# Kernel optimization log

Measured on AMD Instinct MI355X. Metric: run time of the kernel, lower is better.

The kernel has to match this reference:

```python
import jax, jax.numpy as jnp
import numpy as np

N = 100000   # nodes
E = 1600000  # edges
DIN, DH, DOUT = 64, 128, 128


def setup_inputs() -> dict:
    key = jax.random.key(0)
    ks = jax.random.split(key, 12)
    x = jax.random.normal(ks[0], (N, DIN), dtype=jnp.float32)
    edge_index = jax.random.randint(ks[1], (2, E), 0, N, dtype=jnp.int32)
    s = 1.0 / np.sqrt(DIN)
    W1 = jax.random.uniform(ks[2], (DIN, DH), jnp.float32, -s, s)
    b1 = jnp.zeros((DH,), jnp.float32)
    g1 = jnp.ones((DH,), jnp.float32)
    bt1 = jnp.zeros((DH,), jnp.float32)
    s2 = 1.0 / np.sqrt(DH)
    W2 = jax.random.uniform(ks[3], (DH, DOUT), jnp.float32, -s2, s2)
    b2 = jnp.zeros((DOUT,), jnp.float32)
    g2 = jnp.ones((DOUT,), jnp.float32)
    bt2 = jnp.zeros((DOUT,), jnp.float32)
    return {"x": x, "edge_index": edge_index, "W1": W1, "b1": b1, "g1": g1,
            "bt1": bt1, "W2": W2, "b2": b2, "g2": g2, "bt2": bt2}


def _layer_norm(h, g, b, eps=1e-5):
    mu = h.mean(-1, keepdims=True)
    var = h.var(-1, keepdims=True)
    return (h - mu) * jax.lax.rsqrt(var + eps) * g + b


def reference(x, edge_index, W1, b1, g1, bt1, W2, b2, g2, bt2):
    # GCN normalization with self-loops (shared graph structure for both layers)
    src, dst = edge_index[0], edge_index[1]
    loops = jnp.arange(N, dtype=src.dtype)
    src = jnp.concatenate([src, loops])
    dst = jnp.concatenate([dst, loops])
    deg = jax.ops.segment_sum(jnp.ones_like(src, jnp.float32), dst, num_segments=N)
    dinv = jnp.where(deg > 0, jax.lax.rsqrt(deg), 0.0)
    norm = dinv[src] * dinv[dst]  # [E+N]

    def gcn(h, W, b):
        hw = h @ W                         # linear first (PyG GCNConv)
        msg = hw[src] * norm[:, None]      # gather + edge scale
        return jax.ops.segment_sum(msg, dst, num_segments=N) + b

    h = jax.nn.relu(_layer_norm(gcn(x, W1, b1), g1, bt1))
    # dropout is identity at inference
    h = jax.nn.relu(_layer_norm(gcn(h, W2, b2), g2, bt2))
    return h
```

## Files before the change

### kernel.cpp

```cpp
#include <hip/hip_runtime.h>

#define NN 100000
#define NE 1600000
#define NBKT 196
#define CAP 12288
#define EPB 8192
#define ABLK ((NE + EPB - 1) / EPB)
typedef unsigned short u16;
typedef unsigned int u32;

typedef __attribute__((ext_vector_type(8))) short short8v;
typedef __attribute__((ext_vector_type(4))) float f32x4;

__device__ __forceinline__ u32 f2bf(float f) {
    u32 u = __float_as_uint(f);
    return (u + 0x7fffu + ((u >> 16) & 1u)) >> 16;
}
__device__ __forceinline__ u32 pack2(float a, float b) {
    return f2bf(a) | (f2bf(b) << 16);
}
__device__ __forceinline__ void accum8(float* a, uint4 u, float w) {
    a[0] += __uint_as_float(u.x << 16) * w;
    a[1] += __uint_as_float(u.x & 0xffff0000u) * w;
    a[2] += __uint_as_float(u.y << 16) * w;
    a[3] += __uint_as_float(u.y & 0xffff0000u) * w;
    a[4] += __uint_as_float(u.z << 16) * w;
    a[5] += __uint_as_float(u.z & 0xffff0000u) * w;
    a[6] += __uint_as_float(u.w << 16) * w;
    a[7] += __uint_as_float(u.w & 0xffff0000u) * w;
}

__global__ __launch_bounds__(256) void kA_bin(const int* __restrict__ src,
                                              const int* __restrict__ dst,
                                              int* __restrict__ gcnt,
                                              u32* __restrict__ binned) {
    __shared__ int bc[NBKT];
    __shared__ int cbase[NBKT];
    const int tid = threadIdx.x;
    for (int i = tid; i < NBKT; i += 256) bc[i] = 0;
    __syncthreads();
    const int e0 = blockIdx.x * EPB;
#pragma unroll
    for (int i = 0; i < EPB / 256; ++i) {
        const int e = e0 + i * 256 + tid;
        if (e < NE) atomicAdd(&bc[dst[e] >> 9], 1);
    }
    __syncthreads();
    for (int i = tid; i < NBKT; i += 256)
        cbase[i] = bc[i] ? atomicAdd(&gcnt[i], bc[i]) : 0;
    __syncthreads();
    for (int i = tid; i < NBKT; i += 256) bc[i] = 0;
    __syncthreads();
#pragma unroll
    for (int i = 0; i < EPB / 256; ++i) {
        const int e = e0 + i * 256 + tid;
        if (e < NE) {
            const int d = dst[e];
            const int bkt = d >> 9;
            const int p = atomicAdd(&bc[bkt], 1);
            binned[bkt * CAP + cbase[bkt] + p] = ((u32)src[e] << 9) | (u32)(d & 511);
        }
    }
}

__global__ __launch_bounds__(256) void kB_fill(const u32* __restrict__ binned,
                                               const int* __restrict__ gcnt,
                                               int2* __restrict__ off2,
                                               float* __restrict__ dinv,
                                               int* __restrict__ csr) {
    __shared__ int lcnt[512];
    __shared__ int lpos[512];
    __shared__ int ws[4];
    const int b = blockIdx.x;
    const int tid = threadIdx.x;
    const int cnt = gcnt[b];
    const int base0 = b * CAP;
    const int node0 = b << 9;
    lcnt[tid] = 0;
    lcnt[tid + 256] = 0;
    __syncthreads();
    for (int e = tid; e < cnt; e += 256)
        atomicAdd(&lcnt[binned[base0 + e] & 511], 1);
    __syncthreads();
    const int c0 = lcnt[tid * 2], c1 = lcnt[tid * 2 + 1];
    const int s = c0 + c1;
    const int lane = tid & 63, w = tid >> 6;
    int incl = s;
#pragma unroll
    for (int o = 1; o < 64; o <<= 1) {
        const int u = __shfl_up(incl, o);
        if (lane >= o) incl += u;
    }
    if (lane == 63) ws[w] = incl;
    __syncthreads();
    int base = incl - s;
    for (int i = 0; i < w; ++i) base += ws[i];
    lpos[tid * 2] = base;
    lpos[tid * 2 + 1] = base + c0;
    const int n0 = node0 + tid * 2;
    if (n0 < NN) {
        off2[n0] = make_int2(base0 + base, base0 + base + c0);
        dinv[n0] = rsqrtf(1.0f + (float)c0);
    }
    if (n0 + 1 < NN) {
        off2[n0 + 1] = make_int2(base0 + base + c0, base0 + base + c0 + c1);
        dinv[n0 + 1] = rsqrtf(1.0f + (float)c1);
    }
    __syncthreads();
    for (int e = tid; e < cnt; e += 256) {
        const u32 u = binned[base0 + e];
        const int p = atomicAdd(&lpos[u & 511], 1);
        csr[base0 + p] = (int)(u >> 9);
    }
}

__global__ __launch_bounds__(256) void k_prep(const float* __restrict__ W1,
                                              const float* __restrict__ W2,
                                              u16* __restrict__ WT1,
                                              u16* __restrict__ WT2,
                                              int* __restrict__ gcnt) {
    const int i = blockIdx.x * 256 + threadIdx.x;
    if (i < 8192) {
        const int k = i >> 7, c = i & 127;
        WT1[c * 64 + k] = (u16)f2bf(W1[i]);
    } else if (i < 24576) {
        const int i2 = i - 8192;
        const int k = i2 >> 7, c = i2 & 127;
        WT2[c * 128 + k] = (u16)f2bf(W2[i2]);
    } else if (i < 24576 + NBKT) {
        gcnt[i - 24576] = 0;
    }
}

__global__ __launch_bounds__(256) void k_cvt(const float* __restrict__ x,
                                             const float* __restrict__ dinv,
                                             u16* __restrict__ xb) {
    const int i = blockIdx.x * 256 + threadIdx.x;
    if (i < NN * 8) {
        const int row = i >> 3;
        const float dr = dinv[row];
        const float4 v0 = *(const float4*)&x[(size_t)i * 8];
        const float4 v1 = *(const float4*)&x[(size_t)i * 8 + 4];
        uint4 o;
        o.x = pack2(v0.x * dr, v0.y * dr); o.y = pack2(v0.z * dr, v0.w * dr);
        o.z = pack2(v1.x * dr, v1.y * dr); o.w = pack2(v1.z * dr, v1.w * dr);
        *(uint4*)&xb[(size_t)i * 8] = o;
    }
}

__global__ __launch_bounds__(256) void k_agg64(const u16* __restrict__ A,
                                               const int2* __restrict__ off2,
                                               const int* __restrict__ csr,
                                               const float* __restrict__ dinv,
                                               u16* __restrict__ out) {
    const int node = blockIdx.x * 4 + (threadIdx.x >> 6);
    const int lane = threadIdx.x & 63;
    const int sub = lane >> 3, l = lane & 7;
    const char* Ab = (const char*)A + ((u32)l << 4);
    const float di = dinv[node];
    float a[8] = {};
    {
        const uint4 u = *(const uint4*)(Ab + ((u32)node << 7));
        accum8(a, u, (sub == 0) ? 1.0f : 0.0f);
    }
    const int2 oe = off2[node];
    int base = oe.x;
    const int e1 = oe.y;
    u32 iA = 0, iB = 0, iC = 0;
    float vA = 0.f, vB = 0.f, vC = 0.f;
    if (base < e1) {
        const int eA = base + sub, eB = eA + 8, eC = eA + 16;
        iA = (u32)csr[min(eA, e1 - 1)];
        iB = (u32)csr[min(eB, e1 - 1)];
        iC = (u32)csr[min(eC, e1 - 1)];
        vA = (eA < e1) ? 1.f : 0.f;
        vB = (eB < e1) ? 1.f : 0.f;
        vC = (eC < e1) ? 1.f : 0.f;
    }
    while (base < e1) {
        const uint4 uA = *(const uint4*)(Ab + (iA << 7));
        const uint4 uB = *(const uint4*)(Ab + (iB << 7));
        const uint4 uC = *(const uint4*)(Ab + (iC << 7));
        const float wA = vA, wB = vB, wC = vC;
        base += 24;
        if (base < e1) {
            const int eA = base + sub, eB = eA + 8, eC = eA + 16;
            iA = (u32)csr[min(eA, e1 - 1)];
            iB = (u32)csr[min(eB, e1 - 1)];
            iC = (u32)csr[min(eC, e1 - 1)];
            vA = (eA < e1) ? 1.f : 0.f;
            vB = (eB < e1) ? 1.f : 0.f;
            vC = (eC < e1) ? 1.f : 0.f;
        }
        accum8(a, uA, wA);
        accum8(a, uB, wB);
        accum8(a, uC, wC);
    }
#pragma unroll
    for (int i = 0; i < 8; ++i) {
        a[i] += __shfl_xor(a[i], 8);
        a[i] += __shfl_xor(a[i], 16);
        a[i] += __shfl_xor(a[i], 32);
    }
    if (sub == 0) {
        uint4 o;
        o.x = pack2(a[0] * di, a[1] * di); o.y = pack2(a[2] * di, a[3] * di);
        o.z = pack2(a[4] * di, a[5] * di); o.w = pack2(a[6] * di, a[7] * di);
        *(uint4*)((char*)out + ((u32)node << 7) + ((u32)l << 4)) = o;
    }
}

__global__ __launch_bounds__(256) void k_agg128(const u16* __restrict__ A,
                                                const int2* __restrict__ off2,
                                                const int* __restrict__ csr,
                                                const float* __restrict__ dinv,
                                                u16* __restrict__ out) {
    const int node = blockIdx.x * 4 + (threadIdx.x >> 6);
    const int lane = threadIdx.x & 63;
    const int sub = lane >> 4, l = lane & 15;
    const char* Ab = (const char*)A + ((u32)l << 4);
    const float di = dinv[node];
    float a[8] = {};
    {
        const uint4 u = *(const uint4*)(Ab + ((u32)node << 8));
        accum8(a, u, (sub == 0) ? 1.0f : 0.0f);
    }
    const int2 oe = off2[node];
    int base = oe.x;
    const int e1 = oe.y;
    u32 iA = 0, iB = 0, iC = 0;
    float vA = 0.f, vB = 0.f, vC = 0.f;
    if (base < e1) {
        const int eA = base + sub, eB = eA + 4, eC = eA + 8;
        iA = (u32)csr[min(eA, e1 - 1)];
        iB = (u32)csr[min(eB, e1 - 1)];
        iC = (u32)csr[min(eC, e1 - 1)];
        vA = (eA < e1) ? 1.f : 0.f;
        vB = (eB < e1) ? 1.f : 0.f;
        vC = (eC < e1) ? 1.f : 0.f;
    }
    while (base < e1) {
        const uint4 uA = *(const uint4*)(Ab + (iA << 8));
        const uint4 uB = *(const uint4*)(Ab + (iB << 8));
        const uint4 uC = *(const uint4*)(Ab + (iC << 8));
        const float wA = vA, wB = vB, wC = vC;
        base += 12;
        if (base < e1) {
            const int eA = base + sub, eB = eA + 4, eC = eA + 8;
            iA = (u32)csr[min(eA, e1 - 1)];
            iB = (u32)csr[min(eB, e1 - 1)];
            iC = (u32)csr[min(eC, e1 - 1)];
            vA = (eA < e1) ? 1.f : 0.f;
            vB = (eB < e1) ? 1.f : 0.f;
            vC = (eC < e1) ? 1.f : 0.f;
        }
        accum8(a, uA, wA);
        accum8(a, uB, wB);
        accum8(a, uC, wC);
    }
#pragma unroll
    for (int i = 0; i < 8; ++i) {
        a[i] += __shfl_xor(a[i], 16);
        a[i] += __shfl_xor(a[i], 32);
    }
    if (sub == 0) {
        uint4 o;
        o.x = pack2(a[0] * di, a[1] * di); o.y = pack2(a[2] * di, a[3] * di);
        o.z = pack2(a[4] * di, a[5] * di); o.w = pack2(a[6] * di, a[7] * di);
        *(uint4*)((char*)out + ((u32)node << 8) + ((u32)l << 4)) = o;
    }
}

template<int K, bool FP32OUT, bool PRESCALE>
__global__ __launch_bounds__(256) void k_gemm_ln(const u16* __restrict__ Ain,
                                                 const u16* __restrict__ WT,
                                                 const float* __restrict__ bias,
                                                 const float* __restrict__ g,
                                                 const float* __restrict__ bt,
                                                 const float* __restrict__ dinv,
                                                 void* __restrict__ outp) {
    const int tid = threadIdx.x;
    const int wv = tid >> 6, lane = tid & 63;
    const int lr = lane & 15, kg = lane >> 4;
    const int row0 = blockIdx.x * 128 + wv * 32;

    short8v af[2][K / 32];
#pragma unroll
    for (int rt = 0; rt < 2; ++rt) {
        const int r = min(row0 + rt * 16 + lr, NN - 1);
#pragma unroll
        for (int kk = 0; kk < K / 32; ++kk)
            af[rt][kk] = *(const short8v*)&Ain[(size_t)r * K + kk * 32 + kg * 8];
    }
    f32x4 acc[2][8];
#pragma unroll
    for (int rt = 0; rt < 2; ++rt)
#pragma unroll
        for (int nt = 0; nt < 8; ++nt)
            acc[rt][nt] = (f32x4){0.f, 0.f, 0.f, 0.f};

#pragma unroll
    for (int nt = 0; nt < 8; ++nt) {
        const int col = nt * 16 + lr;
        short8v bf[K / 32];
#pragma unroll
        for (int kk = 0; kk < K / 32; ++kk)
            bf[kk] = *(const short8v*)&WT[col * K + kk * 32 + kg * 8];
#pragma unroll
        for (int rt = 0; rt < 2; ++rt)
#pragma unroll
            for (int kk = 0; kk < K / 32; ++kk)
                acc[rt][nt] = __builtin_amdgcn_mfma_f32_16x16x32_bf16(
                    af[rt][kk], bf[kk], acc[rt][nt], 0, 0, 0);
    }

    float bv[8], gv[8], tv[8];
#pragma unroll
    for (int nt = 0; nt < 8; ++nt) {
        const int col = nt * 16 + lr;
        bv[nt] = bias[col]; gv[nt] = g[col]; tv[nt] = bt[col];
    }

#pragma unroll
    for (int rt = 0; rt < 2; ++rt) {
        float s1[4] = {0.f, 0.f, 0.f, 0.f};
        float s2[4] = {0.f, 0.f, 0.f, 0.f};
#pragma unroll
        for (int nt = 0; nt < 8; ++nt)
#pragma unroll
            for (int j = 0; j < 4; ++j) {
                const float v = acc[rt][nt][j] + bv[nt];
                acc[rt][nt][j] = v;
                s1[j] += v;
                s2[j] += v * v;
            }
#pragma unroll
        for (int j = 0; j < 4; ++j)
#pragma unroll
            for (int o = 1; o < 16; o <<= 1) {
                s1[j] += __shfl_xor(s1[j], o);
                s2[j] += __shfl_xor(s2[j], o);
            }
#pragma unroll
        for (int j = 0; j < 4; ++j) {
            const int r = row0 + rt * 16 + kg * 4 + j;
            const float mu = s1[j] * (1.0f / 128.0f);
            const float var = s2[j] * (1.0f / 128.0f) - mu * mu;
            const float rs = rsqrtf(var + 1e-5f);
            if (r < NN) {
                const float dr = PRESCALE ? dinv[r] : 1.0f;
#pragma unroll
                for (int nt = 0; nt < 8; ++nt) {
                    const float y = fmaxf((acc[rt][nt][j] - mu) * rs * gv[nt] + tv[nt], 0.f) * dr;
                    const int col = nt * 16 + lr;
                    if constexpr (FP32OUT)
                        ((float*)outp)[(size_t)r * 128 + col] = y;
                    else
                        ((u16*)outp)[(size_t)r * 128 + col] = (u16)f2bf(y);
                }
            }
        }
    }
}

extern "C" void kernel_launch(void* const* d_in, const int* in_sizes, int n_in,
                              void* d_out, int out_size, void* d_ws, size_t ws_size,
                              hipStream_t stream) {
    const float* x   = (const float*)d_in[0];
    const int*   ei  = (const int*)d_in[1];
    const float* W1  = (const float*)d_in[2];
    const float* b1  = (const float*)d_in[3];
    const float* g1  = (const float*)d_in[4];
    const float* bt1 = (const float*)d_in[5];
    const float* W2  = (const float*)d_in[6];
    const float* b2  = (const float*)d_in[7];
    const float* g2  = (const float*)d_in[8];
    const float* bt2 = (const float*)d_in[9];

    const int* src = ei;
    const int* dst = ei + NE;

    const int NP = (NN + 255) & ~255;
    int*   gcnt  = (int*)d_ws;
    int2*  off2  = (int2*)(gcnt + 256);
    float* dinv  = (float*)(off2 + NP);
    int*   csr   = (int*)(dinv + NP);
    u32*   binR  = (u32*)(csr + NBKT * CAP);
    u16*   xb    = (u16*)(binR + (size_t)NN * 32);
    u16*   aggh  = xb + (size_t)NN * 64;
    u16*   WT1   = aggh + (size_t)NN * 128;
    u16*   WT2   = WT1 + 128 * 64;
    u32*   binned = binR;
    u16*   aggx  = (u16*)binR;
    u16*   h1    = (u16*)d_out;

    k_prep<<<(24576 + NBKT + 255) / 256, 256, 0, stream>>>(W1, W2, WT1, WT2, gcnt);
    kA_bin<<<ABLK, 256, 0, stream>>>(src, dst, gcnt, binned);
    kB_fill<<<NBKT, 256, 0, stream>>>(binned, gcnt, off2, dinv, csr);
    k_cvt<<<(NN * 8 + 255) / 256, 256, 0, stream>>>(x, dinv, xb);

    k_agg64<<<NN / 4, 256, 0, stream>>>(xb, off2, csr, dinv, aggx);
    k_gemm_ln<64, false, true><<<(NN + 127) / 128, 256, 0, stream>>>(
        aggx, WT1, b1, g1, bt1, dinv, h1);

    k_agg128<<<NN / 4, 256, 0, stream>>>(h1, off2, csr, dinv, aggh);
    k_gemm_ln<128, true, false><<<(NN + 127) / 128, 256, 0, stream>>>(
        aggh, WT2, b2, g2, bt2, dinv, d_out);
}
```

Measured before the change: 209.9 us.

## Fuse neighbor aggregation with GEMM and LayerNorm into one kernel per layer

```diff
diff --git a/kernel.cpp b/kernel.cpp
--- a/kernel.cpp
+++ b/kernel.cpp
@@ -148,43 +148,44 @@
     }
 }
 
-__global__ __launch_bounds__(256) void k_agg64(const u16* __restrict__ A,
+template<int K, bool FP32OUT, bool PRESCALE>
+__global__ __launch_bounds__(256) void k_fused(const u16* __restrict__ A,
                                                const int2* __restrict__ off2,
                                                const int* __restrict__ csr,
                                                const float* __restrict__ dinv,
-                                               u16* __restrict__ out) {
-    const int node = blockIdx.x * 4 + (threadIdx.x >> 6);
-    const int lane = threadIdx.x & 63;
-    const int sub = lane >> 3, l = lane & 7;
+                                               const u16* __restrict__ WT,
+                                               const float* __restrict__ bias,
+                                               const float* __restrict__ g,
+                                               const float* __restrict__ bt,
+                                               void* __restrict__ outp) {
+    constexpr int RB = K * 2;
+    constexpr int SUBS = 512 / K;
+    constexpr int LSH = (K == 64) ? 7 : 8;
+    __shared__ u16 As[16 * K];
+    __shared__ float s1s[4][16];
+    __shared__ float s2s[4][16];
+    const int tid = threadIdx.x;
+    const int wv = tid >> 6, lane = tid & 63;
+    const int sub = lane / (64 / SUBS);
+    const int l = lane & (64 / SUBS - 1);
     const char* Ab = (const char*)A + ((u32)l << 4);
-    const float di = dinv[node];
-    float a[8] = {};
-    {
-        const uint4 u = *(const uint4*)(Ab + ((u32)node << 7));
-        accum8(a, u, (sub == 0) ? 1.0f : 0.0f);
-    }
-    const int2 oe = off2[node];
-    int base = oe.x;
-    const int e1 = oe.y;
-    u32 iA = 0, iB = 0, iC = 0;
-    float vA = 0.f, vB = 0.f, vC = 0.f;
-    if (base < e1) {
-        const int eA = base + sub, eB = eA + 8, eC = eA + 16;
-        iA = (u32)csr[min(eA, e1 - 1)];
-        iB = (u32)csr[min(eB, e1 - 1)];
-        iC = (u32)csr[min(eC, e1 - 1)];
-        vA = (eA < e1) ? 1.f : 0.f;
-        vB = (eB < e1) ? 1.f : 0.f;
-        vC = (eC < e1) ? 1.f : 0.f;
-    }
-    while (base < e1) {
-        const uint4 uA = *(const uint4*)(Ab + (iA << 7));
-        const uint4 uB = *(const uint4*)(Ab + (iB << 7));
-        const uint4 uC = *(const uint4*)(Ab + (iC << 7));
-        const float wA = vA, wB = vB, wC = vC;
-        base += 24;
+    const int nodeBase = blockIdx.x * 16 + wv * 4;
+
+    for (int i = 0; i < 4; ++i) {
+        const int node = nodeBase + i;
+        const float di = dinv[node];
+        float a[8] = {};
+        {
+            const uint4 u = *(const uint4*)(Ab + ((u32)node << LSH));
+            accum8(a, u, (sub == 0) ? 1.0f : 0.0f);
+        }
+        const int2 oe = off2[node];
+        int base = oe.x;
+        const int e1 = oe.y;
+        u32 iA = 0, iB = 0, iC = 0;
+        float vA = 0.f, vB = 0.f, vC = 0.f;
         if (base < e1) {
-            const int eA = base + sub, eB = eA + 8, eC = eA + 16;
+            const int eA = base + sub, eB = eA + SUBS, eC = eA + 2 * SUBS;
             iA = (u32)csr[min(eA, e1 - 1)];
             iB = (u32)csr[min(eB, e1 - 1)];
             iC = (u32)csr[min(eC, e1 - 1)];
@@ -192,173 +193,107 @@
             vB = (eB < e1) ? 1.f : 0.f;
             vC = (eC < e1) ? 1.f : 0.f;
         }
-        accum8(a, uA, wA);
-        accum8(a, uB, wB);
-        accum8(a, uC, wC);
-    }
-#pragma unroll
-    for (int i = 0; i < 8; ++i) {
-        a[i] += __shfl_xor(a[i], 8);
-        a[i] += __shfl_xor(a[i], 16);
-        a[i] += __shfl_xor(a[i], 32);
-    }
-    if (sub == 0) {
-        uint4 o;
-        o.x = pack2(a[0] * di, a[1] * di); o.y = pack2(a[2] * di, a[3] * di);
-        o.z = pack2(a[4] * di, a[5] * di); o.w = pack2(a[6] * di, a[7] * di);
-        *(uint4*)((char*)out + ((u32)node << 7) + ((u32)l << 4)) = o;
-    }
-}
-
-__global__ __launch_bounds__(256) void k_agg128(const u16* __restrict__ A,
-                                                const int2* __restrict__ off2,
-                                                const int* __restrict__ csr,
-                                                const float* __restrict__ dinv,
-                                                u16* __restrict__ out) {
-    const int node = blockIdx.x * 4 + (threadIdx.x >> 6);
-    const int lane = threadIdx.x & 63;
-    const int sub = lane >> 4, l = lane & 15;
-    const char* Ab = (const char*)A + ((u32)l << 4);
-    const float di = dinv[node];
-    float a[8] = {};
-    {
-        const uint4 u = *(const uint4*)(Ab + ((u32)node << 8));
-        accum8(a, u, (sub == 0) ? 1.0f : 0.0f);
-    }
-    const int2 oe = off2[node];
-    int base = oe.x;
-    const int e1 = oe.y;
-    u32 iA = 0, iB = 0, iC = 0;
-    float vA = 0.f, vB = 0.f, vC = 0.f;
-    if (base < e1) {
-        const int eA = base + sub, eB = eA + 4, eC = eA + 8;
-        iA = (u32)csr[min(eA, e1 - 1)];
-        iB = (u32)csr[min(eB, e1 - 1)];
-        iC = (u32)csr[min(eC, e1 - 1)];
-        vA = (eA < e1) ? 1.f : 0.f;
-        vB = (eB < e1) ? 1.f : 0.f;
-        vC = (eC < e1) ? 1.f : 0.f;
-    }
-    while (base < e1) {
-        const uint4 uA = *(const uint4*)(Ab + (iA << 8));
-        const uint4 uB = *(const uint4*)(Ab + (iB << 8));
-        const uint4 uC = *(const uint4*)(Ab + (iC << 8));
-        const float wA = vA, wB = vB, wC = vC;
-        base += 12;
-        if (base < e1) {
-            const int eA = base + sub, eB = eA + 4, eC = eA + 8;
-            iA = (u32)csr[min(eA, e1 - 1)];
-            iB = (u32)csr[min(eB, e1 - 1)];
-            iC = (u32)csr[min(eC, e1 - 1)];
-            vA = (eA < e1) ? 1.f : 0.f;
-            vB = (eB < e1) ? 1.f : 0.f;
-            vC = (eC < e1) ? 1.f : 0.f;
-        }
-        accum8(a, uA, wA);
-        accum8(a, uB, wB);
-        accum8(a, uC, wC);
-    }
-#pragma unroll
-    for (int i = 0; i < 8; ++i) {
-        a[i] += __shfl_xor(a[i], 16);
-        a[i] += __shfl_xor(a[i], 32);
-    }
-    if (sub == 0) {
-        uint4 o;
-        o.x = pack2(a[0] * di, a[1] * di); o.y = pack2(a[2] * di, a[3] * di);
-        o.z = pack2(a[4] * di, a[5] * di); o.w = pack2(a[6] * di, a[7] * di);
-        *(uint4*)((char*)out + ((u32)node << 8) + ((u32)l << 4)) = o;
-    }
-}
-
-template<int K, bool FP32OUT, bool PRESCALE>
-__global__ __launch_bounds__(256) void k_gemm_ln(const u16* __restrict__ Ain,
-                                                 const u16* __restrict__ WT,
-                                                 const float* __restrict__ bias,
-                                                 const float* __restrict__ g,
-                                                 const float* __restrict__ bt,
-                                                 const float* __restrict__ dinv,
-                                                 void* __restrict__ outp) {
-    const int tid = threadIdx.x;
-    const int wv = tid >> 6, lane = tid & 63;
+        while (base < e1) {
+            const uint4 uA = *(const uint4*)(Ab + (iA << LSH));
+            const uint4 uB = *(const uint4*)(Ab + (iB << LSH));
+            const uint4 uC = *(const uint4*)(Ab + (iC << LSH));
+            const float wA = vA, wB = vB, wC = vC;
+            base += 3 * SUBS;
+            if (base < e1) {
+                const int eA = base + sub, eB = eA + SUBS, eC = eA + 2 * SUBS;
+                iA = (u32)csr[min(eA, e1 - 1)];
+                iB = (u32)csr[min(eB, e1 - 1)];
+                iC = (u32)csr[min(eC, e1 - 1)];
+                vA = (eA < e1) ? 1.f : 0.f;
+                vB = (eB < e1) ? 1.f : 0.f;
+                vC = (eC < e1) ? 1.f : 0.f;
+            }
+            accum8(a, uA, wA);
+            accum8(a, uB, wB);
+            accum8(a, uC, wC);
+        }
+#pragma unroll
+        for (int t = 0; t < 8; ++t)
+#pragma unroll
+            for (int o = 64 / SUBS; o < 64; o <<= 1)
+                a[t] += __shfl_xor(a[t], o);
+        if (sub == 0) {
+            const int row = wv * 4 + i;
+            uint4 o;
+            o.x = pack2(a[0] * di, a[1] * di); o.y = pack2(a[2] * di, a[3] * di);
+            o.z = pack2(a[4] * di, a[5] * di); o.w = pack2(a[6] * di, a[7] * di);
+            *(uint4*)((char*)As + row * RB + (((u32)l << 4) ^ ((u32)(row & 7) << 4))) = o;
+        }
+    }
+    __syncthreads();
+
     const int lr = lane & 15, kg = lane >> 4;
-    const int row0 = blockIdx.x * 128 + wv * 32;
-
-    short8v af[2][K / 32];
-#pragma unroll
-    for (int rt = 0; rt < 2; ++rt) {
-        const int r = min(row0 + rt * 16 + lr, NN - 1);
-#pragma unroll
-        for (int kk = 0; kk < K / 32; ++kk)
-            af[rt][kk] = *(const short8v*)&Ain[(size_t)r * K + kk * 32 + kg * 8];
-    }
-    f32x4 acc[2][8];
-#pragma unroll
-    for (int rt = 0; rt < 2; ++rt)
-#pragma unroll
-        for (int nt = 0; nt < 8; ++nt)
-            acc[rt][nt] = (f32x4){0.f, 0.f, 0.f, 0.f};
-
-#pragma unroll
-    for (int nt = 0; nt < 8; ++nt) {
-        const int col = nt * 16 + lr;
+    short8v af[K / 32];
+#pragma unroll
+    for (int kk = 0; kk < K / 32; ++kk)
+        af[kk] = *(const short8v*)((const char*)As + lr * RB +
+                                   ((u32)(kk * 64 + kg * 16) ^ ((u32)(lr & 7) << 4)));
+    f32x4 acc[2];
+    float bv[2], gv[2], tv[2];
+#pragma unroll
+    for (int nt = 0; nt < 2; ++nt) {
+        acc[nt] = (f32x4){0.f, 0.f, 0.f, 0.f};
+        const int col = wv * 32 + nt * 16 + lr;
         short8v bf[K / 32];
 #pragma unroll
         for (int kk = 0; kk < K / 32; ++kk)
             bf[kk] = *(const short8v*)&WT[col * K + kk * 32 + kg * 8];
 #pragma unroll
-        for (int rt = 0; rt < 2; ++rt)
-#pragma unroll
-            for (int kk = 0; kk < K / 32; ++kk)
-                acc[rt][nt] = __builtin_amdgcn_mfma_f32_16x16x32_bf16(
-                    af[rt][kk], bf[kk], acc[rt][nt], 0, 0, 0);
-    }
-
-    float bv[8], gv[8], tv[8];
-#pragma unroll
-    for (int nt = 0; nt < 8; ++nt) {
-        const int col = nt * 16 + lr;
+        for (int kk = 0; kk < K / 32; ++kk)
+            acc[nt] = __builtin_amdgcn_mfma_f32_16x16x32_bf16(af[kk], bf[kk], acc[nt], 0, 0, 0);
         bv[nt] = bias[col]; gv[nt] = g[col]; tv[nt] = bt[col];
     }
 
-#pragma unroll
-    for (int rt = 0; rt < 2; ++rt) {
-        float s1[4] = {0.f, 0.f, 0.f, 0.f};
-        float s2[4] = {0.f, 0.f, 0.f, 0.f};
-#pragma unroll
-        for (int nt = 0; nt < 8; ++nt)
-#pragma unroll
-            for (int j = 0; j < 4; ++j) {
-                const float v = acc[rt][nt][j] + bv[nt];
-                acc[rt][nt][j] = v;
-                s1[j] += v;
-                s2[j] += v * v;
-            }
-#pragma unroll
-        for (int j = 0; j < 4; ++j)
-#pragma unroll
-            for (int o = 1; o < 16; o <<= 1) {
-                s1[j] += __shfl_xor(s1[j], o);
-                s2[j] += __shfl_xor(s2[j], o);
-            }
+    float s1[4] = {0.f, 0.f, 0.f, 0.f};
+    float s2[4] = {0.f, 0.f, 0.f, 0.f};
+#pragma unroll
+    for (int nt = 0; nt < 2; ++nt)
 #pragma unroll
         for (int j = 0; j < 4; ++j) {
-            const int r = row0 + rt * 16 + kg * 4 + j;
-            const float mu = s1[j] * (1.0f / 128.0f);
-            const float var = s2[j] * (1.0f / 128.0f) - mu * mu;
-            const float rs = rsqrtf(var + 1e-5f);
-            if (r < NN) {
-                const float dr = PRESCALE ? dinv[r] : 1.0f;
-#pragma unroll
-                for (int nt = 0; nt < 8; ++nt) {
-                    const float y = fmaxf((acc[rt][nt][j] - mu) * rs * gv[nt] + tv[nt], 0.f) * dr;
-                    const int col = nt * 16 + lr;
-                    if constexpr (FP32OUT)
-                        ((float*)outp)[(size_t)r * 128 + col] = y;
-                    else
-                        ((u16*)outp)[(size_t)r * 128 + col] = (u16)f2bf(y);
-                }
-            }
+            const float v = acc[nt][j] + bv[nt];
+            acc[nt][j] = v;
+            s1[j] += v;
+            s2[j] += v * v;
+        }
+#pragma unroll
+    for (int j = 0; j < 4; ++j)
+#pragma unroll
+        for (int o = 1; o < 16; o <<= 1) {
+            s1[j] += __shfl_xor(s1[j], o);
+            s2[j] += __shfl_xor(s2[j], o);
+        }
+    if (lr == 0) {
+#pragma unroll
+        for (int j = 0; j < 4; ++j) {
+            s1s[wv][kg * 4 + j] = s1[j];
+            s2s[wv][kg * 4 + j] = s2[j];
+        }
+    }
+    __syncthreads();
+
+#pragma unroll
+    for (int j = 0; j < 4; ++j) {
+        const int row = kg * 4 + j;
+        const float t1 = s1s[0][row] + s1s[1][row] + s1s[2][row] + s1s[3][row];
+        const float t2 = s2s[0][row] + s2s[1][row] + s2s[2][row] + s2s[3][row];
+        const float mu = t1 * (1.0f / 128.0f);
+        const float var = t2 * (1.0f / 128.0f) - mu * mu;
+        const float rs = rsqrtf(var + 1e-5f);
+        const int node = blockIdx.x * 16 + row;
+        const float dr = PRESCALE ? dinv[node] : 1.0f;
+#pragma unroll
+        for (int nt = 0; nt < 2; ++nt) {
+            const float y = fmaxf((acc[nt][j] - mu) * rs * gv[nt] + tv[nt], 0.f) * dr;
+            const int col = wv * 32 + nt * 16 + lr;
+            if constexpr (FP32OUT)
+                ((float*)outp)[(size_t)node * 128 + col] = y;
+            else
+                ((u16*)outp)[(size_t)node * 128 + col] = (u16)f2bf(y);
         }
     }
 }
@@ -381,29 +316,24 @@
     const int* dst = ei + NE;
 
     const int NP = (NN + 255) & ~255;
-    int*   gcnt  = (int*)d_ws;
-    int2*  off2  = (int2*)(gcnt + 256);
-    float* dinv  = (float*)(off2 + NP);
-    int*   csr   = (int*)(dinv + NP);
-    u32*   binR  = (u32*)(csr + NBKT * CAP);
-    u16*   xb    = (u16*)(binR + (size_t)NN * 32);
-    u16*   aggh  = xb + (size_t)NN * 64;
-    u16*   WT1   = aggh + (size_t)NN * 128;
-    u16*   WT2   = WT1 + 128 * 64;
-    u32*   binned = binR;
-    u16*   aggx  = (u16*)binR;
-    u16*   h1    = (u16*)d_out;
+    int*   gcnt   = (int*)d_ws;
+    int2*  off2   = (int2*)(gcnt + 256);
+    float* dinv   = (float*)(off2 + NP);
+    int*   csr    = (int*)(dinv + NP);
+    u32*   binned = (u32*)(csr + NBKT * CAP);
+    u16*   xb     = (u16*)(binned + NBKT * CAP);
+    u16*   h1     = xb + (size_t)NN * 64;
+    u16*   WT1    = h1 + (size_t)NN * 128;
+    u16*   WT2    = WT1 + 128 * 64;
 
     k_prep<<<(24576 + NBKT + 255) / 256, 256, 0, stream>>>(W1, W2, WT1, WT2, gcnt);
     kA_bin<<<ABLK, 256, 0, stream>>>(src, dst, gcnt, binned);
     kB_fill<<<NBKT, 256, 0, stream>>>(binned, gcnt, off2, dinv, csr);
     k_cvt<<<(NN * 8 + 255) / 256, 256, 0, stream>>>(x, dinv, xb);
 
-    k_agg64<<<NN / 4, 256, 0, stream>>>(xb, off2, csr, dinv, aggx);
-    k_gemm_ln<64, false, true><<<(NN + 127) / 128, 256, 0, stream>>>(
-        aggx, WT1, b1, g1, bt1, dinv, h1);
-
-    k_agg128<<<NN / 4, 256, 0, stream>>>(h1, off2, csr, dinv, aggh);
-    k_gemm_ln<128, true, false><<<(NN + 127) / 128, 256, 0, stream>>>(
-        aggh, WT2, b2, g2, bt2, dinv, d_out);
-}
+    k_fused<64, false, true><<<NN / 16, 256, 0, stream>>>(
+        xb, off2, csr, dinv, WT1, b1, g1, bt1, h1);
+
+    k_fused<128, true, false><<<NN / 16, 256, 0, stream>>>(
+        h1, off2, csr, dinv, WT2, b2, g2, bt2, d_out);
+}
```

Result: faster. 204.7 us (-2.5%).
